# Kernel tuning notes

Hardware: AMD Instinct MI355X
Metric: run time of the kernel (lower is better)

The kernel has to match this reference:

```python
import jax, jax.numpy as jnp
import numpy as np

N_NODES = 50000
N_EDGES = 800000
D = 64
STEPS = 10
NEG_SLOPE = 0.2


def setup_inputs() -> dict:
    key = jax.random.key(0)
    ks = jax.random.split(key, 9)
    x = jax.random.normal(ks[0], (N_NODES, D), dtype=jnp.float32)
    edge_index_l1 = jax.random.randint(ks[1], (2, N_EDGES), 0, N_NODES, dtype=jnp.int64 if jax.config.jax_enable_x64 else jnp.int32)
    edge_index_l2 = jax.random.randint(ks[2], (2, N_EDGES), 0, N_NODES, dtype=jnp.int64 if jax.config.jax_enable_x64 else jnp.int32)
    s = 1.0 / np.sqrt(D)
    W1 = jax.random.normal(ks[3], (D, D), dtype=jnp.float32) * s
    a1_src = jax.random.normal(ks[4], (D,), dtype=jnp.float32) * s
    a1_dst = jax.random.normal(ks[5], (D,), dtype=jnp.float32) * s
    W2 = jax.random.normal(ks[6], (D, D), dtype=jnp.float32) * s
    a2_src = jax.random.normal(ks[7], (D,), dtype=jnp.float32) * s
    a2_dst = jax.random.normal(ks[8], (D,), dtype=jnp.float32) * s
    return {
        "x": x,
        "edge_index_l1": edge_index_l1,
        "edge_index_l2": edge_index_l2,
        "W1": W1, "a1_src": a1_src, "a1_dst": a1_dst,
        "W2": W2, "a2_src": a2_src, "a2_dst": a2_dst,
    }


def _gat_layer(x, src, dst, W, a_src, a_dst):
    """Single-head GATConv: out_i = sum_{j->i} softmax_i(LeakyReLU(a_s.Wx_j + a_d.Wx_i)) * Wx_j."""
    h = x @ W                                            # [N, D]
    e = jax.nn.leaky_relu((h @ a_src)[src] + (h @ a_dst)[dst], NEG_SLOPE)  # [E]
    # numerically stable segment softmax over incoming edges of each dst node
    m = jax.ops.segment_max(e, dst, num_segments=N_NODES)
    m = jax.lax.stop_gradient(jnp.where(jnp.isfinite(m), m, 0.0))
    w = jnp.exp(e - m[dst])                              # [E]
    denom = jax.ops.segment_sum(w, dst, num_segments=N_NODES)
    att = w / (denom[dst] + 1e-16)                       # [E]
    return jax.ops.segment_sum(h[src] * att[:, None], dst, num_segments=N_NODES)


def _base_operator(xt, ei1, ei2, W1, a1_src, a1_dst, W2, a2_src, a2_dst):
    h = _gat_layer(xt, ei1[0], ei1[1], W1, a1_src, a1_dst)
    h = jax.nn.elu(h)
    return _gat_layer(h, ei2[0], ei2[1], W2, a2_src, a2_dst)


def reference(x, edge_index_l1, edge_index_l2, W1, a1_src, a1_dst, W2, a2_src, a2_dst):
    ts = jnp.linspace(0.0, 1.0, STEPS, dtype=x.dtype)    # [STEPS]
    h_step = ts[1] - ts[0]                               # trapezoid-like uniform weight

    def step(acc, t):
        out = _base_operator(x * t, edge_index_l1, edge_index_l2,
                             W1, a1_src, a1_dst, W2, a2_src, a2_dst)
        return acc + out, None

    result, _ = jax.lax.scan(step, jnp.zeros_like(x), ts)
    return result * h_step
```

## Files before the change

kernel.cpp:

```cpp
#include <hip/hip_runtime.h>
#include <hip/hip_bf16.h>

#define NN 50000
#define NE 800000
#define DD 64
#define NEG 0.2f
#define NB (NN / 4)
#define EG4B ((NE / 4 + 255) / 256)

#define RFL(x) __builtin_amdgcn_readfirstlane(x)
typedef unsigned short u16;

__global__ __launch_bounds__(256) void k_fat1(
    const int* __restrict__ dst1, const int* __restrict__ dst2,
    int* __restrict__ cnt1, int* __restrict__ cnt2,
    int* __restrict__ rank1, int* __restrict__ rank2,
    const float* __restrict__ x, const float* __restrict__ W1,
    const float* __restrict__ a1s, const float* __restrict__ a1d,
    _Float16* __restrict__ H1h, float* __restrict__ al1s, float* __restrict__ al1d,
    const float* __restrict__ W2, const float* __restrict__ a2s,
    const float* __restrict__ a2d, float* __restrict__ t2s, float* __restrict__ t2d) {
    const int bid = blockIdx.x;
    if (bid < EG4B) {
        int t = bid * 256 + threadIdx.x;
        if (t < NE / 4) {
            int4 d1 = ((const int4*)dst1)[t];
            int4 d2 = ((const int4*)dst2)[t];
            int4 r1, r2;
            r1.x = atomicAdd(&cnt1[d1.x], 1); r1.y = atomicAdd(&cnt1[d1.y], 1);
            r1.z = atomicAdd(&cnt1[d1.z], 1); r1.w = atomicAdd(&cnt1[d1.w], 1);
            r2.x = atomicAdd(&cnt2[d2.x], 1); r2.y = atomicAdd(&cnt2[d2.y], 1);
            r2.z = atomicAdd(&cnt2[d2.z], 1); r2.w = atomicAdd(&cnt2[d2.w], 1);
            ((int4*)rank1)[t] = r1;
            ((int4*)rank2)[t] = r2;
        }
    } else if (bid < EG4B + NB) {
        const int lane = threadIdx.x & 63;
        const int i = (bid - EG4B) * 4 + (threadIdx.x >> 6);
        const float xv = x[i * DD + lane];
        float h = 0.f;
#pragma unroll
        for (int j = 0; j < DD; ++j) h = fmaf(__shfl(xv, j), W1[j * DD + lane], h);
        H1h[(size_t)i * DD + lane] = (_Float16)h;
        float ps = h * a1s[lane], pd = h * a1d[lane];
#pragma unroll
        for (int o = 32; o; o >>= 1) { ps += __shfl_xor(ps, o); pd += __shfl_xor(pd, o); }
        if (lane == 0) { al1s[i] = ps; al1d[i] = pd; }
    } else {
        if (threadIdx.x < DD) {
            int j = threadIdx.x;
            float ss = 0.f, sd = 0.f;
#pragma unroll
            for (int d = 0; d < DD; ++d) {
                float w = W2[j * DD + d];
                ss = fmaf(w, a2s[d], ss);
                sd = fmaf(w, a2d[d], sd);
            }
            t2s[j] = ss;
            t2d[j] = sd;
        }
    }
}

__global__ __launch_bounds__(1024) void k_scan(const int* __restrict__ cnt1, int* __restrict__ off1,
                                               const int* __restrict__ cnt2, int* __restrict__ off2) {
    const int* cnt = blockIdx.x ? cnt2 : cnt1;
    int* off = blockIdx.x ? off2 : off1;
    __shared__ int lds[1024];
    const int tid = threadIdx.x;
    const int CH = (NN + 1023) / 1024;
    const int base = tid * CH;
    int s = 0;
    for (int q = 0; q < CH; ++q) {
        int idx = base + q;
        if (idx < NN) s += cnt[idx];
    }
    lds[tid] = s;
    __syncthreads();
    for (int d = 1; d < 1024; d <<= 1) {
        int v = (tid >= d) ? lds[tid - d] : 0;
        __syncthreads();
        lds[tid] += v;
        __syncthreads();
    }
    int run = tid ? lds[tid - 1] : 0;
    for (int q = 0; q < CH; ++q) {
        int idx = base + q;
        if (idx < NN) { off[idx] = run; run += cnt[idx]; }
    }
    if (tid == 1023) off[NN] = lds[1023];
}

__device__ __forceinline__ void place_body(int t, const int* __restrict__ src,
                                           const int* __restrict__ dst,
                                           const int* __restrict__ off,
                                           const int* __restrict__ rank,
                                           u16* __restrict__ csr) {
    if (t < NE / 4) {
        int4 s = ((const int4*)src)[t];
        int4 d = ((const int4*)dst)[t];
        int4 r = ((const int4*)rank)[t];
        csr[off[d.x] + r.x] = (u16)s.x;
        csr[off[d.y] + r.y] = (u16)s.y;
        csr[off[d.z] + r.z] = (u16)s.z;
        csr[off[d.w] + r.w] = (u16)s.w;
    }
}

__global__ void k_place1(const int* __restrict__ src, const int* __restrict__ dst,
                         const int* __restrict__ off, const int* __restrict__ rank,
                         u16* __restrict__ csr) {
    place_body(blockIdx.x * blockDim.x + threadIdx.x, src, dst, off, rank, csr);
}

__global__ __launch_bounds__(256) void k_fat2(
    const int* __restrict__ src2, const int* __restrict__ dst2,
    const int* __restrict__ off2, const int* __restrict__ rank2, u16* __restrict__ csr2,
    const int* __restrict__ off, const u16* __restrict__ csrc,
    const float* __restrict__ al1s, const float* __restrict__ al1d,
    const _Float16* __restrict__ H1h,
    const float* __restrict__ t2s, const float* __restrict__ t2d,
    uint4* __restrict__ H2a, _Float16* __restrict__ H2b,
    float* __restrict__ al2s8, float* __restrict__ al2s9, float* __restrict__ al2d) {
    __shared__ int2 lsr[4][64];
    const int bid = blockIdx.x;
    if (bid < EG4B) {
        place_body(bid * 256 + threadIdx.x, src2, dst2, off2, rank2, csr2);
        return;
    }
    const int lane = threadIdx.x & 63;
    const int wid = threadIdx.x >> 6;
    const int i = (bid - EG4B) * 4 + wid;
    const int p0 = RFL(off[i]);
    const int p1 = RFL(off[i + 1]);
    const float adv = al1d[i];
    float num[9], den[9];
#pragma unroll
    for (int k = 0; k < 9; ++k) { num[k] = 0.f; den[k] = 0.f; }

    for (int base = p0; base < p1; base += 64) {
        int m = p1 - base; if (m > 64) m = 64;
        int sv = 0; float rv = 0.f;
        if (lane < m) {
            sv = csrc[base + lane];
            float z = al1s[sv] + adv;
            float c = z > 0.f ? z : NEG * z;
            rv = __expf(c * (1.f / 9.f));
        }
        {
            float w = rv;
#pragma unroll
            for (int k = 0; k < 9; ++k) { den[k] += w; w *= rv; }
        }
        lsr[wid][lane] = make_int2(sv, __float_as_int(rv));
        asm volatile("s_waitcnt lgkmcnt(0)" ::: "memory");
        int j = 0;
        for (; j + 3 < m; j += 4) {
            int2 e0 = lsr[wid][j], e1 = lsr[wid][j + 1];
            int2 e2 = lsr[wid][j + 2], e3 = lsr[wid][j + 3];
            float h0 = (float)H1h[(size_t)e0.x * DD + lane];
            float h1v = (float)H1h[(size_t)e1.x * DD + lane];
            float h2v = (float)H1h[(size_t)e2.x * DD + lane];
            float h3v = (float)H1h[(size_t)e3.x * DD + lane];
            float r0 = __int_as_float(e0.y), r1 = __int_as_float(e1.y);
            float r2 = __int_as_float(e2.y), r3 = __int_as_float(e3.y);
            float w0 = r0, w1 = r1, w2 = r2, w3 = r3;
#pragma unroll
            for (int k = 0; k < 9; ++k) {
                num[k] = fmaf(w0, h0, num[k]);  w0 *= r0;
                num[k] = fmaf(w1, h1v, num[k]); w1 *= r1;
                num[k] = fmaf(w2, h2v, num[k]); w2 *= r2;
                num[k] = fmaf(w3, h3v, num[k]); w3 *= r3;
            }
        }
        for (; j < m; ++j) {
            int2 e0 = lsr[wid][j];
            float h0 = (float)H1h[(size_t)e0.x * DD + lane];
            float r0 = __int_as_float(e0.y);
            float w0 = r0;
#pragma unroll
            for (int k = 0; k < 9; ++k) { num[k] = fmaf(w0, h0, num[k]); w0 *= r0; }
        }
    }
#pragma unroll
    for (int k = 0; k < 9; ++k) {
#pragma unroll
        for (int o = 32; o; o >>= 1) den[k] += __shfl_xor(den[k], o);
    }

    const float tss = t2s[lane];
    const float tdd = t2d[lane];
    float hm[9];
#pragma unroll
    for (int k = 0; k < 9; ++k) {
        float t = (float)(k + 1) * (1.f / 9.f);
        float v = (den[k] > 0.f) ? (t * num[k] / den[k]) : 0.f;
        hm[k] = (v > 0.f) ? v : expm1f(v);
    }
#pragma unroll
    for (int k = 0; k < 9; ++k) {
        float ps = hm[k] * tss, pd = hm[k] * tdd;
#pragma unroll
        for (int o = 32; o; o >>= 1) { ps += __shfl_xor(ps, o); pd += __shfl_xor(pd, o); }
        if (lane == 0) {
            if (k < 8) al2s8[(size_t)i * 8 + k] = ps;
            else       al2s9[i] = ps;
            al2d[(size_t)i * 9 + k] = pd;
        }
    }
    union { _Float16 h[8]; uint4 u; } pk;
#pragma unroll
    for (int k = 0; k < 8; ++k) pk.h[k] = (_Float16)hm[k];
    H2a[(size_t)i * DD + lane] = pk.u;
    H2b[(size_t)i * DD + lane] = (_Float16)hm[8];
}

__global__ __launch_bounds__(256) void k_l2(
    const int* __restrict__ off, const u16* __restrict__ csrc,
    const float* __restrict__ al2s8, const float* __restrict__ al2s9,
    const float* __restrict__ al2d,
    const uint4* __restrict__ H2a, const _Float16* __restrict__ H2b,
    const float* __restrict__ W2, float* __restrict__ out) {
    __shared__ float lw[4][64][12];
    const int lane = threadIdx.x & 63;
    const int wid = threadIdx.x >> 6;
    const int i = blockIdx.x * 4 + wid;
    const int p0 = RFL(off[i]);
    const int p1 = RFL(off[i + 1]);
    float adv[9];
#pragma unroll
    for (int k = 0; k < 9; ++k) adv[k] = al2d[(size_t)i * 9 + k];
    float num[9], den[9];
#pragma unroll
    for (int k = 0; k < 9; ++k) { num[k] = 0.f; den[k] = 0.f; }

    for (int base = p0; base < p1; base += 64) {
        int m = p1 - base; if (m > 64) m = 64;
        int sv = 0; float wv[9];
#pragma unroll
        for (int k = 0; k < 9; ++k) wv[k] = 0.f;
        if (lane < m) {
            sv = csrc[base + lane];
            const float4* pa = (const float4*)(al2s8 + (size_t)sv * 8);
            float4 A0 = pa[0], A1 = pa[1];
            float as[9] = {A0.x, A0.y, A0.z, A0.w, A1.x, A1.y, A1.z, A1.w, al2s9[sv]};
#pragma unroll
            for (int k = 0; k < 9; ++k) {
                float z = as[k] + adv[k];
                float lr = z > 0.f ? z : NEG * z;
                wv[k] = __expf(lr);
            }
        }
#pragma unroll
        for (int k = 0; k < 9; ++k) den[k] += wv[k];
        float* dst = &lw[wid][lane][0];
        *(float4*)dst       = make_float4(wv[0], wv[1], wv[2], wv[3]);
        *(float4*)(dst + 4) = make_float4(wv[4], wv[5], wv[6], wv[7]);
        dst[8] = wv[8];
        dst[9] = __int_as_float(sv);
        asm volatile("s_waitcnt lgkmcnt(0)" ::: "memory");
        int j = 0;
        for (; j + 1 < m; j += 2) {
            const float* s0 = &lw[wid][j][0];
            const float* s1 = &lw[wid][j + 1][0];
            int sj0 = __float_as_int(s0[9]);
            int sj1 = __float_as_int(s1[9]);
            union { uint4 v; _Float16 h[8]; } c0, c1;
            c0.v = H2a[(size_t)sj0 * DD + lane];
            c1.v = H2a[(size_t)sj1 * DD + lane];
            float h90 = (float)H2b[(size_t)sj0 * DD + lane];
            float h91 = (float)H2b[(size_t)sj1 * DD + lane];
            float4 wA0 = *(const float4*)s0, wB0 = *(const float4*)(s0 + 4);
            float4 wA1 = *(const float4*)s1, wB1 = *(const float4*)(s1 + 4);
            num[0] = fmaf(wA0.x, (float)c0.h[0], num[0]);
            num[1] = fmaf(wA0.y, (float)c0.h[1], num[1]);
            num[2] = fmaf(wA0.z, (float)c0.h[2], num[2]);
            num[3] = fmaf(wA0.w, (float)c0.h[3], num[3]);
            num[4] = fmaf(wB0.x, (float)c0.h[4], num[4]);
            num[5] = fmaf(wB0.y, (float)c0.h[5], num[5]);
            num[6] = fmaf(wB0.z, (float)c0.h[6], num[6]);
            num[7] = fmaf(wB0.w, (float)c0.h[7], num[7]);
            num[8] = fmaf(s0[8], h90, num[8]);
            num[0] = fmaf(wA1.x, (float)c1.h[0], num[0]);
            num[1] = fmaf(wA1.y, (float)c1.h[1], num[1]);
            num[2] = fmaf(wA1.z, (float)c1.h[2], num[2]);
            num[3] = fmaf(wA1.w, (float)c1.h[3], num[3]);
            num[4] = fmaf(wB1.x, (float)c1.h[4], num[4]);
            num[5] = fmaf(wB1.y, (float)c1.h[5], num[5]);
            num[6] = fmaf(wB1.z, (float)c1.h[6], num[6]);
            num[7] = fmaf(wB1.w, (float)c1.h[7], num[7]);
            num[8] = fmaf(s1[8], h91, num[8]);
        }
        if (j < m) {
            const float* s0 = &lw[wid][j][0];
            int sj0 = __float_as_int(s0[9]);
            union { uint4 v; _Float16 h[8]; } c0;
            c0.v = H2a[(size_t)sj0 * DD + lane];
            float h90 = (float)H2b[(size_t)sj0 * DD + lane];
            float4 wA0 = *(const float4*)s0, wB0 = *(const float4*)(s0 + 4);
            num[0] = fmaf(wA0.x, (float)c0.h[0], num[0]);
            num[1] = fmaf(wA0.y, (float)c0.h[1], num[1]);
            num[2] = fmaf(wA0.z, (float)c0.h[2], num[2]);
            num[3] = fmaf(wA0.w, (float)c0.h[3], num[3]);
            num[4] = fmaf(wB0.x, (float)c0.h[4], num[4]);
            num[5] = fmaf(wB0.y, (float)c0.h[5], num[5]);
            num[6] = fmaf(wB0.z, (float)c0.h[6], num[6]);
            num[7] = fmaf(wB0.w, (float)c0.h[7], num[7]);
            num[8] = fmaf(s0[8], h90, num[8]);
        }
    }
#pragma unroll
    for (int k = 0; k < 9; ++k) {
#pragma unroll
        for (int o = 32; o; o >>= 1) den[k] += __shfl_xor(den[k], o);
    }
    float vsum = 0.f;
#pragma unroll
    for (int k = 0; k < 9; ++k) vsum += (den[k] > 0.f) ? (num[k] / den[k]) : 0.f;
    float h2 = 0.f;
#pragma unroll 8
    for (int j = 0; j < DD; ++j) h2 = fmaf(__shfl(vsum, j), W2[j * DD + lane], h2);
    out[(size_t)i * DD + lane] = h2 * (1.f / 9.f);
}

extern "C" void kernel_launch(void* const* d_in, const int* in_sizes, int n_in,
                              void* d_out, int out_size, void* d_ws, size_t ws_size,
                              hipStream_t stream) {
    const float* x   = (const float*)d_in[0];
    const int*   ei1 = (const int*)d_in[1];
    const int*   ei2 = (const int*)d_in[2];
    const float* W1  = (const float*)d_in[3];
    const float* a1s = (const float*)d_in[4];
    const float* a1d = (const float*)d_in[5];
    const float* W2  = (const float*)d_in[6];
    const float* a2s = (const float*)d_in[7];
    const float* a2d = (const float*)d_in[8];
    float* out = (float*)d_out;

    const int* src1 = ei1;
    const int* dst1 = ei1 + NE;
    const int* src2 = ei2;
    const int* dst2 = ei2 + NE;

    uint4* H2a    = (uint4*)d_ws;
    _Float16* H1h = (_Float16*)((float*)d_ws + (size_t)NN * 256);
    float* al1s   = (float*)H1h + (size_t)NN * DD / 2;
    float* al1d   = al1s + NN;
    float* al2s8  = al1d + NN;
    float* al2s9  = al2s8 + (size_t)NN * 8;
    float* al2d   = al2s9 + NN;
    _Float16* H2b = (_Float16*)(al2d + (size_t)NN * 9);
    int* rank1 = (int*)((float*)H2b + (size_t)NN * DD / 2);
    int* rank2 = rank1 + NE;
    u16* csr1  = (u16*)(rank2 + NE);
    u16* csr2  = csr1 + NE;
    float* t2s = (float*)(csr2 + NE);
    float* t2d = t2s + DD;
    int* off1 = (int*)(t2d + DD);
    int* off2 = off1 + (NN + 1);
    int* cnt1 = off2 + (NN + 1);
    int* cnt2 = cnt1 + NN;

    hipMemsetAsync(cnt1, 0, 2 * NN * sizeof(int), stream);
    k_fat1<<<EG4B + NB + 1, 256, 0, stream>>>(
        dst1, dst2, cnt1, cnt2, rank1, rank2,
        x, W1, a1s, a1d, H1h, al1s, al1d,
        W2, a2s, a2d, t2s, t2d);
    k_scan<<<2, 1024, 0, stream>>>(cnt1, off1, cnt2, off2);
    k_place1<<<EG4B, 256, 0, stream>>>(src1, dst1, off1, rank1, csr1);
    k_fat2<<<EG4B + NB, 256, 0, stream>>>(
        src2, dst2, off2, rank2, csr2,
        off1, csr1, al1s, al1d, H1h, t2s, t2d,
        H2a, H2b, al2s8, al2s9, al2d);
    k_l2<<<NB, 256, 0, stream>>>(off2, csr2, al2s8, al2s9, al2d, H2a, H2b, W2, out);
}
```

Before: 458.3 us.

## Gather packed half2 H1 rows so each half-wave processes a different edge

H1 is now stored as packed pairs of fp16 values in 32-bit words. In the layer-1 aggregation each 32-lane half of the wave gathers a full 128-byte row for a different edge, so two edges are processed per gather step instead of one. Each lane keeps two sets of accumulators, and a cross-half shuffle plus a redistribution shuffle at the end restore the per-lane feature layout. The intent is to halve the number of gather instructions and widen each memory access. In exchange it adds accumulator registers, extra shuffles, and a tail loop that relies on the padded LDS entries for odd edge counts.

```diff
diff --git a/kernel.cpp b/kernel.cpp
--- a/kernel.cpp
+++ b/kernel.cpp
@@ -17,7 +17,7 @@
     int* __restrict__ rank1, int* __restrict__ rank2,
     const float* __restrict__ x, const float* __restrict__ W1,
     const float* __restrict__ a1s, const float* __restrict__ a1d,
-    _Float16* __restrict__ H1h, float* __restrict__ al1s, float* __restrict__ al1d,
+    unsigned int* __restrict__ H1u, float* __restrict__ al1s, float* __restrict__ al1d,
     const float* __restrict__ W2, const float* __restrict__ a2s,
     const float* __restrict__ a2d, float* __restrict__ t2s, float* __restrict__ t2d) {
     const int bid = blockIdx.x;
@@ -41,7 +41,14 @@
         float h = 0.f;
 #pragma unroll
         for (int j = 0; j < DD; ++j) h = fmaf(__shfl(xv, j), W1[j * DD + lane], h);
-        H1h[(size_t)i * DD + lane] = (_Float16)h;
+        float hlo = __shfl(h, (lane & 31) * 2);
+        float hhi = __shfl(h, (lane & 31) * 2 + 1);
+        if (lane < 32) {
+            union { unsigned int u; _Float16 hh[2]; } pk2;
+            pk2.hh[0] = (_Float16)hlo;
+            pk2.hh[1] = (_Float16)hhi;
+            H1u[(size_t)i * 32 + lane] = pk2.u;
+        }
         float ps = h * a1s[lane], pd = h * a1d[lane];
 #pragma unroll
         for (int o = 32; o; o >>= 1) { ps += __shfl_xor(ps, o); pd += __shfl_xor(pd, o); }
@@ -118,7 +125,7 @@
     const int* __restrict__ off2, const int* __restrict__ rank2, u16* __restrict__ csr2,
     const int* __restrict__ off, const u16* __restrict__ csrc,
     const float* __restrict__ al1s, const float* __restrict__ al1d,
-    const _Float16* __restrict__ H1h,
+    const unsigned int* __restrict__ H1u,
     const float* __restrict__ t2s, const float* __restrict__ t2d,
     uint4* __restrict__ H2a, _Float16* __restrict__ H2b,
     float* __restrict__ al2s8, float* __restrict__ al2s9, float* __restrict__ al2d) {
@@ -130,13 +137,15 @@
     }
     const int lane = threadIdx.x & 63;
     const int wid = threadIdx.x >> 6;
+    const int half = lane >> 5;
+    const int q = lane & 31;
     const int i = (bid - EG4B) * 4 + wid;
     const int p0 = RFL(off[i]);
     const int p1 = RFL(off[i + 1]);
     const float adv = al1d[i];
-    float num[9], den[9];
-#pragma unroll
-    for (int k = 0; k < 9; ++k) { num[k] = 0.f; den[k] = 0.f; }
+    float numx[9], numy[9], den[9];
+#pragma unroll
+    for (int k = 0; k < 9; ++k) { numx[k] = 0.f; numy[k] = 0.f; den[k] = 0.f; }
 
     for (int base = p0; base < p1; base += 64) {
         int m = p1 - base; if (m > 64) m = 64;
@@ -155,32 +164,49 @@
         lsr[wid][lane] = make_int2(sv, __float_as_int(rv));
         asm volatile("s_waitcnt lgkmcnt(0)" ::: "memory");
         int j = 0;
-        for (; j + 3 < m; j += 4) {
-            int2 e0 = lsr[wid][j], e1 = lsr[wid][j + 1];
-            int2 e2 = lsr[wid][j + 2], e3 = lsr[wid][j + 3];
-            float h0 = (float)H1h[(size_t)e0.x * DD + lane];
-            float h1v = (float)H1h[(size_t)e1.x * DD + lane];
-            float h2v = (float)H1h[(size_t)e2.x * DD + lane];
-            float h3v = (float)H1h[(size_t)e3.x * DD + lane];
-            float r0 = __int_as_float(e0.y), r1 = __int_as_float(e1.y);
-            float r2 = __int_as_float(e2.y), r3 = __int_as_float(e3.y);
-            float w0 = r0, w1 = r1, w2 = r2, w3 = r3;
+        for (; j + 7 < m; j += 8) {
+            int2 eA = lsr[wid][j     + half];
+            int2 eB = lsr[wid][j + 2 + half];
+            int2 eC = lsr[wid][j + 4 + half];
+            int2 eD = lsr[wid][j + 6 + half];
+            unsigned int uA = H1u[(size_t)eA.x * 32 + q];
+            unsigned int uB = H1u[(size_t)eB.x * 32 + q];
+            unsigned int uC = H1u[(size_t)eC.x * 32 + q];
+            unsigned int uD = H1u[(size_t)eD.x * 32 + q];
+            float rA = __int_as_float(eA.y), rB = __int_as_float(eB.y);
+            float rC = __int_as_float(eC.y), rD = __int_as_float(eD.y);
+            union { unsigned int u; _Float16 h[2]; } cA, cB, cC, cD;
+            cA.u = uA; cB.u = uB; cC.u = uC; cD.u = uD;
+            float hAx = (float)cA.h[0], hAy = (float)cA.h[1];
+            float hBx = (float)cB.h[0], hBy = (float)cB.h[1];
+            float hCx = (float)cC.h[0], hCy = (float)cC.h[1];
+            float hDx = (float)cD.h[0], hDy = (float)cD.h[1];
+            float wA = rA, wB = rB, wC = rC, wD = rD;
 #pragma unroll
             for (int k = 0; k < 9; ++k) {
-                num[k] = fmaf(w0, h0, num[k]);  w0 *= r0;
-                num[k] = fmaf(w1, h1v, num[k]); w1 *= r1;
-                num[k] = fmaf(w2, h2v, num[k]); w2 *= r2;
-                num[k] = fmaf(w3, h3v, num[k]); w3 *= r3;
+                numx[k] = fmaf(wA, hAx, numx[k]); numy[k] = fmaf(wA, hAy, numy[k]); wA *= rA;
+                numx[k] = fmaf(wB, hBx, numx[k]); numy[k] = fmaf(wB, hBy, numy[k]); wB *= rB;
+                numx[k] = fmaf(wC, hCx, numx[k]); numy[k] = fmaf(wC, hCy, numy[k]); wC *= rC;
+                numx[k] = fmaf(wD, hDx, numx[k]); numy[k] = fmaf(wD, hDy, numy[k]); wD *= rD;
             }
         }
-        for (; j < m; ++j) {
-            int2 e0 = lsr[wid][j];
-            float h0 = (float)H1h[(size_t)e0.x * DD + lane];
-            float r0 = __int_as_float(e0.y);
-            float w0 = r0;
-#pragma unroll
-            for (int k = 0; k < 9; ++k) { num[k] = fmaf(w0, h0, num[k]); w0 *= r0; }
-        }
+        for (; j < m; j += 2) {
+            int2 e = lsr[wid][j + half];
+            unsigned int u = H1u[(size_t)e.x * 32 + q];
+            float r = __int_as_float(e.y);
+            union { unsigned int uu; _Float16 h[2]; } c; c.uu = u;
+            float hx = (float)c.h[0], hy = (float)c.h[1];
+            float w = r;
+#pragma unroll
+            for (int k = 0; k < 9; ++k) {
+                numx[k] = fmaf(w, hx, numx[k]); numy[k] = fmaf(w, hy, numy[k]); w *= r;
+            }
+        }
+    }
+#pragma unroll
+    for (int k = 0; k < 9; ++k) {
+        numx[k] += __shfl_xor(numx[k], 32);
+        numy[k] += __shfl_xor(numy[k], 32);
     }
 #pragma unroll
     for (int k = 0; k < 9; ++k) {
@@ -193,8 +219,11 @@
     float hm[9];
 #pragma unroll
     for (int k = 0; k < 9; ++k) {
+        float a = __shfl(numx[k], lane >> 1);
+        float b = __shfl(numy[k], lane >> 1);
+        float nm = (lane & 1) ? b : a;
         float t = (float)(k + 1) * (1.f / 9.f);
-        float v = (den[k] > 0.f) ? (t * num[k] / den[k]) : 0.f;
+        float v = (den[k] > 0.f) ? (t * nm / den[k]) : 0.f;
         hm[k] = (v > 0.f) ? v : expm1f(v);
     }
 #pragma unroll
@@ -343,8 +372,8 @@
     const int* dst2 = ei2 + NE;
 
     uint4* H2a    = (uint4*)d_ws;
-    _Float16* H1h = (_Float16*)((float*)d_ws + (size_t)NN * 256);
-    float* al1s   = (float*)H1h + (size_t)NN * DD / 2;
+    unsigned int* H1u = (unsigned int*)((float*)d_ws + (size_t)NN * 256);
+    float* al1s   = (float*)H1u + (size_t)NN * 32;
     float* al1d   = al1s + NN;
     float* al2s8  = al1d + NN;
     float* al2s9  = al2s8 + (size_t)NN * 8;
@@ -364,13 +393,13 @@
     hipMemsetAsync(cnt1, 0, 2 * NN * sizeof(int), stream);
     k_fat1<<<EG4B + NB + 1, 256, 0, stream>>>(
         dst1, dst2, cnt1, cnt2, rank1, rank2,
-        x, W1, a1s, a1d, H1h, al1s, al1d,
+        x, W1, a1s, a1d, H1u, al1s, al1d,
         W2, a2s, a2d, t2s, t2d);
     k_scan<<<2, 1024, 0, stream>>>(cnt1, off1, cnt2, off2);
     k_place1<<<EG4B, 256, 0, stream>>>(src1, dst1, off1, rank1, csr1);
     k_fat2<<<EG4B + NB, 256, 0, stream>>>(
         src2, dst2, off2, rank2, csr2,
-        off1, csr1, al1s, al1d, H1h, t2s, t2d,
+        off1, csr1, al1s, al1d, H1u, t2s, t2d,
         H2a, H2b, al2s8, al2s9, al2d);
     k_l2<<<NB, 256, 0, stream>>>(off2, csr2, al2s8, al2s9, al2d, H2a, H2b, W2, out);
 }
```

New measurement: 475.0 us. +3.6%, slower.
